# Optimization experiments

Measured on AMD Instinct MI355X. Metric: run time of the kernel, lower is better.

The kernel has to match this reference:

```python
import jax, jax.numpy as jnp
import numpy as np

B, N, D = 8, 2048, 512

def setup_inputs() -> dict:
    key = jax.random.key(0)
    ks = jax.random.split(key, 8)
    s = 1.0 / np.sqrt(D)
    return {
        "inputs": jax.random.normal(ks[0], (B, N, D), dtype=jnp.float32),
        "mask": jnp.ones((B, N), dtype=jnp.int32),
        "Wk": jax.random.normal(ks[1], (D, D), dtype=jnp.float32) * s,
        "bk": jax.random.normal(ks[2], (D,), dtype=jnp.float32) * s,
        "Wq": jax.random.normal(ks[3], (D, D), dtype=jnp.float32) * s,
        "bq": jax.random.normal(ks[4], (D,), dtype=jnp.float32) * s,
        "Wv": jax.random.normal(ks[5], (D, D), dtype=jnp.float32) * s,
        "bv": jax.random.normal(ks[6], (D,), dtype=jnp.float32) * s,
    }

def reference(inputs, mask, Wk, bk, Wq, bq, Wv, bv):
    # torch Linear: y = x @ W.T + b
    keys = jnp.einsum('bnd,ed->bne', inputs, Wk) + bk
    queries = jnp.einsum('bnd,ed->bne', inputs, Wq) + bq
    values = jnp.einsum('bnd,ed->bne', inputs, Wv) + bv
    norm = jnp.sqrt(jnp.asarray(D, inputs.dtype))
    scores = jnp.einsum('bqd,bkd->bqk', queries, keys) / norm  # [B,N,N]
    scores = jnp.where(mask[:, None, :] == 0, jnp.asarray(-1e9, scores.dtype), scores)
    attn = jax.nn.softmax(scores, axis=-1)
    return jnp.einsum('bqk,bkd->bqd', attn, values)
```

## Files before the change

kernel.cpp:

```cpp
#include <hip/hip_runtime.h>
#include <hip/hip_bf16.h>


typedef __attribute__((ext_vector_type(8))) short short8;
typedef __attribute__((ext_vector_type(4))) float f32x4;

#define DEV __device__ __forceinline__
#define GLOBAL_AS __attribute__((address_space(1)))
#define LDS_AS __attribute__((address_space(3)))

static DEV ushort f2bs(float f) {
  union { float f; unsigned u; } x; x.f = f;
  unsigned r = (x.u + 0x7fffu + ((x.u >> 16) & 1u)) >> 16;
  return (ushort)r;
}

static DEV f32x4 mfma16(short8 a, short8 b, f32x4 c) {
  return __builtin_amdgcn_mfma_f32_16x16x32_bf16(a, b, c, 0, 0, 0);
}

static DEV void async16(const void* g, void* l) {
  __builtin_amdgcn_global_load_lds((const GLOBAL_AS void*)g, (LDS_AS void*)l, 16, 0, 0);
}

__global__ void convert_all(const float* __restrict__ wq, const float* __restrict__ wk,
                            const float* __restrict__ wv, const float* __restrict__ x,
                            ushort* __restrict__ wb, ushort* __restrict__ xb,
                            float* __restrict__ lde) {
  int i = blockIdx.x * 256 + threadIdx.x;
  if (i >= 2293760) {
    int off = (i - 2293760) * 4;
    float4 z; z.x = 0.f; z.y = 0.f; z.z = 0.f; z.w = 0.f;
    *(float4*)(lde + off) = z;
    return;
  }
  const float* src;
  ushort* dst;
  if (i < 196608) {
    int which = i >> 16;
    int off = (i & 65535) * 4;
    src = ((which == 0) ? wq : (which == 1) ? wk : wv) + off;
    dst = wb + (size_t)which * 262144 + off;
  } else {
    int off = (i - 196608) * 4;
    src = x + off;
    dst = xb + off;
  }
  float4 v = *(const float4*)src;
  ushort4 o;
  o.x = f2bs(v.x); o.y = f2bs(v.y); o.z = f2bs(v.z); o.w = f2bs(v.w);
  *(ushort4*)dst = o;
}

#define KLOOP_STAGE(Aptr, lda, Bptr, ldb)                                      \
  do {                                                                         \
    _Pragma("unroll")                                                          \
    for (int t = 0; t < 8; t++) {                                              \
      int rowbase = (t & 3) * 32 + wave * 8;                                   \
      int r = rowbase + (lane >> 3);                                           \
      int gc = (lane & 7) ^ (r & 7);                                           \
      if (t < 4)                                                               \
        async16((Aptr) + (size_t)(rowblk * 128 + r) * (lda) + kb + gc * 8,     \
                &As[rowbase * 64]);                                            \
      else                                                                     \
        async16((Bptr) + (size_t)(colblk * 128 + r) * (ldb) + kb + gc * 8,     \
                &Bs[rowbase * 64]);                                            \
    }                                                                          \
  } while (0)

#define KLOOP_MFMA()                                                           \
  do {                                                                         \
    _Pragma("unroll")                                                          \
    for (int ks = 0; ks < 2; ks++) {                                           \
      short8 af[4], bfr[4];                                                    \
      _Pragma("unroll")                                                        \
      for (int t = 0; t < 4; t++) {                                            \
        int ra = wm * 64 + t * 16 + c16;                                       \
        int rb = wn * 64 + t * 16 + c16;                                       \
        af[t]  = *(const short8*)&As[ra * 64 + (((ks * 4 + quad) ^ (ra & 7)) * 8)]; \
        bfr[t] = *(const short8*)&Bs[rb * 64 + (((ks * 4 + quad) ^ (rb & 7)) * 8)]; \
      }                                                                        \
      _Pragma("unroll")                                                        \
      for (int mt = 0; mt < 4; mt++)                                           \
        _Pragma("unroll")                                                      \
        for (int nt = 0; nt < 4; nt++)                                         \
          acc[mt][nt] = mfma16(af[mt], bfr[nt], acc[mt][nt]);                  \
    }                                                                          \
  } while (0)

__launch_bounds__(256, 4)
__global__ void qkv_gemm(const ushort* __restrict__ Xb, const ushort* __restrict__ Wb,
                         const float* __restrict__ bq, const float* __restrict__ bk,
                         const float* __restrict__ bv,
                         ushort* __restrict__ Qb, ushort* __restrict__ Kb,
                         ushort* __restrict__ Vtb) {
  const int rowblk = blockIdx.x;
  const int colblk = blockIdx.y;
  const int z = colblk >> 2;

  __shared__ ushort S[2 * 128 * 64];
  ushort* As = S;
  ushort* Bs = S + 128 * 64;

  const int tid = threadIdx.x;
  const int wave = tid >> 6, lane = tid & 63, quad = lane >> 4, c16 = lane & 15;
  const int wm = wave & 1, wn = wave >> 1;

  f32x4 acc[4][4];
#pragma unroll
  for (int mt = 0; mt < 4; mt++)
#pragma unroll
    for (int nt = 0; nt < 4; nt++) acc[mt][nt] = (f32x4)0.0f;

  for (int kb = 0; kb < 512; kb += 64) {
    __syncthreads();
    KLOOP_STAGE(Xb, 512, Wb, 512);
    __syncthreads();
    KLOOP_MFMA();
  }

  const float* bias = (z == 0) ? bq : (z == 1) ? bk : bv;
  float bvals[4];
#pragma unroll
  for (int nt = 0; nt < 4; nt++) {
    int eg = colblk * 128 + wn * 64 + nt * 16 + c16;
    bvals[nt] = bias[eg & 511];
  }
  const float sc = (z == 0) ? 0.044194173824159216f : 1.0f;

  const int row0 = rowblk * 128 + wm * 64;
  const int col0 = colblk * 128 + wn * 64;
  if (z < 2) {
    ushort* O = (z == 0) ? Qb : Kb;
#pragma unroll
    for (int mt = 0; mt < 4; mt++)
#pragma unroll
      for (int nt = 0; nt < 4; nt++) {
        int el = (col0 + nt * 16 + c16) & 511;
#pragma unroll
        for (int r = 0; r < 4; r++) {
          int n = row0 + mt * 16 + quad * 4 + r;
          O[(size_t)n * 512 + el] = f2bs((acc[mt][nt][r] + bvals[nt]) * sc);
        }
      }
  } else {
    __syncthreads();
    ushort* T = S;
#pragma unroll
    for (int nt = 0; nt < 4; nt++) {
      int ell = wn * 64 + nt * 16 + c16;
#pragma unroll
      for (int mt = 0; mt < 4; mt++) {
        int n0l = wm * 64 + mt * 16 + quad * 4;
        ushort4 o;
        o.x = f2bs(acc[mt][nt][0] + bvals[nt]);
        o.y = f2bs(acc[mt][nt][1] + bvals[nt]);
        o.z = f2bs(acc[mt][nt][2] + bvals[nt]);
        o.w = f2bs(acc[mt][nt][3] + bvals[nt]);
        *(ushort4*)&T[ell * 128 + (((n0l >> 3) ^ (ell & 15)) << 3) + (n0l & 4)] = o;
      }
    }
    __syncthreads();
    const int c4 = tid & 3, er = tid >> 2;
    const int bb = rowblk >> 4;
    const int nbase = (rowblk & 15) * 128;
    const int elbase = (colblk & 3) * 128;
#pragma unroll
    for (int part = 0; part < 2; part++) {
      int ell = part * 64 + er;
      size_t ge = ((size_t)bb * 512 + elbase + ell) * 2048;
#pragma unroll
      for (int j2 = 0; j2 < 4; j2++) {
        int n0 = j2 * 32 + c4 * 8;
        short8 v = *(short8*)&T[ell * 128 + (((n0 >> 3) ^ (ell & 15)) << 3)];
        __builtin_nontemporal_store(v, (short8*)(Vtb + ge + nbase + n0));
      }
    }
  }
}

__launch_bounds__(256, 4)
__global__ void gemm_s(const ushort* __restrict__ Kb, const ushort* __restrict__ Qb,
                       const int* __restrict__ mask, ushort* __restrict__ Pm,
                       float* __restrict__ l) {
  const int bid = blockIdx.x;
  const int b = bid & 7;
  const int rowblk = (bid >> 3) & 15;
  const int colblk = bid >> 7;
  const ushort* A  = Kb + (size_t)b * 2048 * 512;
  const ushort* Bq = Qb + (size_t)b * 2048 * 512;

  __shared__ ushort S[2 * 128 * 64];
  ushort* As = S;
  ushort* Bs = S + 128 * 64;

  const int tid = threadIdx.x;
  const int wave = tid >> 6, lane = tid & 63, quad = lane >> 4, c16 = lane & 15;
  const int wm = wave & 1, wn = wave >> 1;

  f32x4 acc[4][4];
#pragma unroll
  for (int mt = 0; mt < 4; mt++)
#pragma unroll
    for (int nt = 0; nt < 4; nt++) acc[mt][nt] = (f32x4)0.0f;

  for (int kb = 0; kb < 512; kb += 64) {
    __syncthreads();
    KLOOP_STAGE(A, 512, Bq, 512);
    __syncthreads();
    KLOOP_MFMA();
  }

  const int row0 = rowblk * 128 + wm * 64;
  const int col0 = colblk * 128 + wn * 64;
  float lpart[4] = {0.0f, 0.0f, 0.0f, 0.0f};

  __syncthreads();
  ushort* T = S;
#pragma unroll
  for (int mt = 0; mt < 4; mt++) {
    int key0 = row0 + mt * 16 + quad * 4;
    int k0l  = wm * 64 + mt * 16 + quad * 4;
    int4 mv = *(const int4*)&mask[b * 2048 + key0];
    float mf0 = mv.x ? 1.0f : 0.0f, mf1 = mv.y ? 1.0f : 0.0f;
    float mf2 = mv.z ? 1.0f : 0.0f, mf3 = mv.w ? 1.0f : 0.0f;
#pragma unroll
    for (int nt = 0; nt < 4; nt++) {
      int ql = wn * 64 + nt * 16 + c16;
      float p0 = __expf(acc[mt][nt][0]) * mf0;
      float p1 = __expf(acc[mt][nt][1]) * mf1;
      float p2 = __expf(acc[mt][nt][2]) * mf2;
      float p3 = __expf(acc[mt][nt][3]) * mf3;
      ushort4 o;
      o.x = f2bs(p0); o.y = f2bs(p1); o.z = f2bs(p2); o.w = f2bs(p3);
      *(ushort4*)&T[ql * 128 + (((k0l >> 3) ^ (ql & 15)) << 3) + (k0l & 4)] = o;
      lpart[nt] += p0 + p1 + p2 + p3;
    }
  }
#pragma unroll
  for (int nt = 0; nt < 4; nt++) {
    float v = lpart[nt];
    v += __shfl_xor(v, 16, 64);
    v += __shfl_xor(v, 32, 64);
    if (quad == 0) atomicAdd(&l[b * 2048 + col0 + nt * 16 + c16], v);
  }
  __syncthreads();
  {
    const int c4 = tid & 3, er = tid >> 2;
#pragma unroll
    for (int part = 0; part < 2; part++) {
      int ql = part * 64 + er;
      size_t gq = ((size_t)b * 2048 + colblk * 128 + ql) * 2048;
#pragma unroll
      for (int j2 = 0; j2 < 4; j2++) {
        int n0 = j2 * 32 + c4 * 8;
        short8 v = *(short8*)&T[ql * 128 + (((n0 >> 3) ^ (ql & 15)) << 3)];
        __builtin_nontemporal_store(v, (short8*)(Pm + gq + rowblk * 128 + n0));
      }
    }
  }
}

#define PH_ST_A(pp, kt, rd)                                                    \
  do {                                                                         \
    int rowbase_ = (rd) * 64 + wave * 8;                                       \
    int r_ = rowbase_ + (lane >> 3);                                           \
    int gc_ = (lane & 7) ^ (r_ & 7);                                           \
    async16(gA + (size_t)(arow0 + r_) * glda + (kt) * 64 + gc_ * 8,            \
            SdA + (pp) * 16384 + rowbase_ * 64);                               \
  } while (0)

#define PH_ST_B(pp, kt, rd)                                                    \
  do {                                                                         \
    int rowbase_ = (rd) * 64 + wave * 8;                                       \
    int r_ = rowbase_ + (lane >> 3);                                           \
    int gc_ = (lane & 7) ^ (r_ & 7);                                           \
    async16(gB + (size_t)(brow0 + r_) * gldb + (kt) * 64 + gc_ * 8,            \
            SdB + (pp) * 8192 + rowbase_ * 64);                                \
  } while (0)

#define PH_READ(pp, ks, afx, bfx)                                              \
  do {                                                                         \
    const ushort* Ap_ = SdA + (pp) * 16384;                                    \
    const ushort* Bp_ = SdB + (pp) * 8192;                                     \
    _Pragma("unroll")                                                          \
    for (int mf = 0; mf < 4; mf++) {                                           \
      int ra = wm * 64 + mf * 16 + c16;                                        \
      afx[mf] = *(const short8*)&Ap_[ra * 64 + ((((ks)*4 + quad) ^ (ra & 7)) * 8)]; \
    }                                                                          \
    _Pragma("unroll")                                                          \
    for (int nf = 0; nf < 4; nf++) {                                           \
      int rb = wn * 64 + nf * 16 + c16;                                        \
      bfx[nf] = *(const short8*)&Bp_[rb * 64 + ((((ks)*4 + quad) ^ (rb & 7)) * 8)]; \
    }                                                                          \
  } while (0)

#define PH_MFMA(afx, bfx, h)                                                   \
  do {                                                                         \
    __builtin_amdgcn_s_setprio(1);                                             \
    _Pragma("unroll")                                                          \
    for (int mf = (h) * 2; mf < (h) * 2 + 2; mf++)                             \
      _Pragma("unroll")                                                        \
      for (int nf = 0; nf < 4; nf++)                                           \
        acc[mf][nf] = mfma16(afx[mf], bfx[nf], acc[mf][nf]);                   \
    __builtin_amdgcn_s_setprio(0);                                             \
  } while (0)

#define PH_TILE(pp, kt, dostage)                                               \
  do {                                                                         \
    PH_READ(pp, 0, af0, bf0);                                                  \
    __builtin_amdgcn_s_barrier();                                              \
    asm volatile("s_waitcnt lgkmcnt(0)" ::: "memory");                         \
    __builtin_amdgcn_sched_barrier(0);                                         \
    PH_MFMA(af0, bf0, 0);                                                      \
    __builtin_amdgcn_s_barrier();                                              \
    PH_READ(pp, 1, af1, bf1);                                                  \
    __builtin_amdgcn_s_barrier();                                              \
    asm volatile("s_waitcnt lgkmcnt(0)" ::: "memory");                         \
    __builtin_amdgcn_sched_barrier(0);                                         \
    PH_MFMA(af0, bf0, 1);                                                      \
    __builtin_amdgcn_s_barrier();         \
    if (dostage) { PH_ST_A(pp, (kt) + 2, 0); PH_ST_A(pp, (kt) + 2, 1);         \
                   PH_ST_A(pp, (kt) + 2, 2); }                                 \
    PH_MFMA(af1, bf1, 0);                                                      \
    __builtin_amdgcn_s_barrier();                                              \
    if (dostage) { PH_ST_A(pp, (kt) + 2, 3); PH_ST_B(pp, (kt) + 2, 0);         \
                   PH_ST_B(pp, (kt) + 2, 1); }                                 \
    PH_MFMA(af1, bf1, 1);                                                      \
    if (dostage) { asm volatile("s_waitcnt vmcnt(6)" ::: "memory"); }          \
    else         { asm volatile("s_waitcnt vmcnt(0)" ::: "memory"); }          \
    __builtin_amdgcn_sched_barrier(0);                                         \
    __builtin_amdgcn_s_barrier();        \
  } while (0)

#define PH_PROLOGUE()                                                          \
  do {                                                                         \
    PH_ST_A(0, 0, 0); PH_ST_A(0, 0, 1); PH_ST_A(0, 0, 2); PH_ST_A(0, 0, 3);    \
    PH_ST_B(0, 0, 0); PH_ST_B(0, 0, 1);                                        \
    PH_ST_A(1, 1, 0); PH_ST_A(1, 1, 1); PH_ST_A(1, 1, 2); PH_ST_A(1, 1, 3);    \
    PH_ST_B(1, 1, 0); PH_ST_B(1, 1, 1);                                        \
    asm volatile("s_waitcnt vmcnt(6)" ::: "memory");                           \
    __builtin_amdgcn_sched_barrier(0);                                         \
    __builtin_amdgcn_s_barrier();                                              \
  } while (0)

__launch_bounds__(512, 2)
__global__ void gemm_o(const ushort* __restrict__ Pm, const ushort* __restrict__ Vtb,
                       const float* __restrict__ l, float* __restrict__ out) {
  const int bid = blockIdx.x;
  const int b = bid & 7;
  const int rowblk = (bid >> 3) & 7;
  const int colblk = bid >> 6;

  extern __shared__ ushort Sd[];
  ushort* SdA = Sd;
  ushort* SdB = Sd + 32768;

  const int tid = threadIdx.x;
  const int wave = tid >> 6, lane = tid & 63, quad = lane >> 4, c16 = lane & 15;
  const int wm = wave >> 1, wn = wave & 1;

  const ushort* gA = Pm + (size_t)b * 2048 * 2048;  const int glda = 2048;
  const int arow0 = rowblk * 256;
  const ushort* gB = Vtb + (size_t)b * 512 * 2048;  const int gldb = 2048;
  const int brow0 = colblk * 128;

  f32x4 acc[4][4];
#pragma unroll
  for (int mf = 0; mf < 4; mf++)
#pragma unroll
    for (int nf = 0; nf < 4; nf++) acc[mf][nf] = (f32x4)0.0f;

  PH_PROLOGUE();
  short8 af0[4], bf0[4], af1[4], bf1[4];
  for (int i = 0; i < 16; i++) {
    const int ds = (i < 15);
    PH_TILE(0, 2 * i, ds);
    PH_TILE(1, 2 * i + 1, ds);
  }

  const int row0 = rowblk * 256 + wm * 64;
  const int col0 = colblk * 128 + wn * 64;
  float linv[4][4];
#pragma unroll
  for (int mf = 0; mf < 4; mf++)
#pragma unroll
    for (int r = 0; r < 4; r++)
      linv[mf][r] = 1.0f / l[b * 2048 + row0 + mf * 16 + quad * 4 + r];
#pragma unroll
  for (int mf = 0; mf < 4; mf++)
#pragma unroll
    for (int nf = 0; nf < 4; nf++) {
      int col = col0 + nf * 16 + c16;
#pragma unroll
      for (int r = 0; r < 4; r++) {
        int row = row0 + mf * 16 + quad * 4 + r;
        out[((size_t)b * 2048 + row) * 512 + col] = acc[mf][nf][r] * linv[mf][r];
      }
    }
}

extern "C" void kernel_launch(void* const* d_in, const int* in_sizes, int n_in,
                              void* d_out, int out_size, void* d_ws, size_t ws_size,
                              hipStream_t stream) {
  (void)in_sizes; (void)n_in; (void)out_size; (void)ws_size;
  const float* X    = (const float*)d_in[0];
  const int*   mask = (const int*)d_in[1];
  const float* Wk   = (const float*)d_in[2];
  const float* bk   = (const float*)d_in[3];
  const float* Wq   = (const float*)d_in[4];
  const float* bq   = (const float*)d_in[5];
  const float* Wv   = (const float*)d_in[6];
  const float* bv   = (const float*)d_in[7];
  float* out = (float*)d_out;

  ushort* ws  = (ushort*)d_ws;
  ushort* Pm  = ws;
  ushort* Xb  = ws;
  ushort* Wb  = ws + (size_t)33554432;
  ushort* Qb  = Wb + (size_t)786432;
  ushort* Kb  = Qb + (size_t)8388608;
  ushort* Vtb = Kb + (size_t)8388608;
  float*  lde = (float*)(Vtb + (size_t)8388608);

  convert_all<<<8976, 256, 0, stream>>>(Wq, Wk, Wv, X, Wb, Xb, lde);
  qkv_gemm<<<dim3(128, 12), 256, 0, stream>>>(Xb, Wb, bq, bk, bv, Qb, Kb, Vtb);
  gemm_s<<<2048, 256, 0, stream>>>(Kb, Qb, mask, Pm, lde);
  gemm_o<<<256, 512, 98304, stream>>>(Pm, Vtb, lde, out);
}
```

Baseline: 197.4 us.

## Triple-buffer LDS pipeline in output GEMM with deeper prefetch

Converts the gemm_o main loop from double to triple buffering in shared memory, prefetching tile k+3 instead of k+2. It adds a three-stage prologue, unrolled loop tail handling and a final tile with no barrier. The intent is to hide more global-load latency behind MFMA work. In exchange, dynamic LDS grows to 144KB, which limits residency to one block per CU.

```diff
diff --git a/kernel.cpp b/kernel.cpp
--- a/kernel.cpp
+++ b/kernel.cpp
@@ -306,7 +306,10 @@
     __builtin_amdgcn_s_setprio(0);                                             \
   } while (0)
 
-#define PH_TILE(pp, kt, dostage)                                               \
+#define PH_WAIT_(N) asm volatile("s_waitcnt vmcnt(" #N ")" ::: "memory")
+#define PH_WAIT(N) PH_WAIT_(N)
+
+#define PH_TILE3(pp, kt, dostage, WN)                                          \
   do {                                                                         \
     PH_READ(pp, 0, af0, bf0);                                                  \
     __builtin_amdgcn_s_barrier();                                              \
@@ -320,26 +323,43 @@
     __builtin_amdgcn_sched_barrier(0);                                         \
     PH_MFMA(af0, bf0, 1);                                                      \
     __builtin_amdgcn_s_barrier();         \
-    if (dostage) { PH_ST_A(pp, (kt) + 2, 0); PH_ST_A(pp, (kt) + 2, 1);         \
-                   PH_ST_A(pp, (kt) + 2, 2); }                                 \
+    if (dostage) { PH_ST_A(pp, (kt) + 3, 0); PH_ST_A(pp, (kt) + 3, 1);         \
+                   PH_ST_A(pp, (kt) + 3, 2); }                                 \
     PH_MFMA(af1, bf1, 0);                                                      \
     __builtin_amdgcn_s_barrier();                                              \
-    if (dostage) { PH_ST_A(pp, (kt) + 2, 3); PH_ST_B(pp, (kt) + 2, 0);         \
-                   PH_ST_B(pp, (kt) + 2, 1); }                                 \
+    if (dostage) { PH_ST_A(pp, (kt) + 3, 3); PH_ST_B(pp, (kt) + 3, 0);         \
+                   PH_ST_B(pp, (kt) + 3, 1); }                                 \
     PH_MFMA(af1, bf1, 1);                                                      \
-    if (dostage) { asm volatile("s_waitcnt vmcnt(6)" ::: "memory"); }          \
-    else         { asm volatile("s_waitcnt vmcnt(0)" ::: "memory"); }          \
+    PH_WAIT(WN);                                                               \
     __builtin_amdgcn_sched_barrier(0);                                         \
     __builtin_amdgcn_s_barrier();        \
   } while (0)
 
-#define PH_PROLOGUE()                                                          \
+#define PH_TILE3_LAST(pp)                                                      \
+  do {                                                                         \
+    PH_READ(pp, 0, af0, bf0);                                                  \
+    __builtin_amdgcn_s_barrier();                                              \
+    asm volatile("s_waitcnt lgkmcnt(0)" ::: "memory");                         \
+    __builtin_amdgcn_sched_barrier(0);                                         \
+    PH_MFMA(af0, bf0, 0);                                                      \
+    __builtin_amdgcn_s_barrier();                                              \
+    PH_READ(pp, 1, af1, bf1);                                                  \
+    asm volatile("s_waitcnt lgkmcnt(0)" ::: "memory");                         \
+    __builtin_amdgcn_sched_barrier(0);                                         \
+    PH_MFMA(af0, bf0, 1);                                                      \
+    PH_MFMA(af1, bf1, 0);                                                      \
+    PH_MFMA(af1, bf1, 1);                                                      \
+  } while (0)
+
+#define PH_PROLOGUE3()                                                         \
   do {                                                                         \
     PH_ST_A(0, 0, 0); PH_ST_A(0, 0, 1); PH_ST_A(0, 0, 2); PH_ST_A(0, 0, 3);    \
     PH_ST_B(0, 0, 0); PH_ST_B(0, 0, 1);                                        \
     PH_ST_A(1, 1, 0); PH_ST_A(1, 1, 1); PH_ST_A(1, 1, 2); PH_ST_A(1, 1, 3);    \
     PH_ST_B(1, 1, 0); PH_ST_B(1, 1, 1);                                        \
-    asm volatile("s_waitcnt vmcnt(6)" ::: "memory");                           \
+    PH_ST_A(2, 2, 0); PH_ST_A(2, 2, 1); PH_ST_A(2, 2, 2); PH_ST_A(2, 2, 3);    \
+    PH_ST_B(2, 2, 0); PH_ST_B(2, 2, 1);                                        \
+    PH_WAIT(12);                                                               \
     __builtin_amdgcn_sched_barrier(0);                                         \
     __builtin_amdgcn_s_barrier();                                              \
   } while (0)
@@ -354,7 +374,7 @@
 
   extern __shared__ ushort Sd[];
   ushort* SdA = Sd;
-  ushort* SdB = Sd + 32768;
+  ushort* SdB = Sd + 3 * 16384;
 
   const int tid = threadIdx.x;
   const int wave = tid >> 6, lane = tid & 63, quad = lane >> 4, c16 = lane & 15;
@@ -371,13 +391,18 @@
 #pragma unroll
     for (int nf = 0; nf < 4; nf++) acc[mf][nf] = (f32x4)0.0f;
 
-  PH_PROLOGUE();
+  PH_PROLOGUE3();
   short8 af0[4], bf0[4], af1[4], bf1[4];
-  for (int i = 0; i < 16; i++) {
-    const int ds = (i < 15);
-    PH_TILE(0, 2 * i, ds);
-    PH_TILE(1, 2 * i + 1, ds);
-  }
+  for (int i = 0; i < 9; i++) {
+    PH_TILE3(0, 3 * i,     1, 12);
+    PH_TILE3(1, 3 * i + 1, 1, 12);
+    PH_TILE3(2, 3 * i + 2, 1, 12);
+  }
+  PH_TILE3(0, 27, 1, 12);
+  PH_TILE3(1, 28, 1, 12);
+  PH_TILE3(2, 29, 0, 6);
+  PH_TILE3(0, 30, 0, 0);
+  PH_TILE3_LAST(1);
 
   const int row0 = rowblk * 256 + wm * 64;
   const int col0 = colblk * 128 + wn * 64;
@@ -426,5 +451,5 @@
   convert_all<<<8976, 256, 0, stream>>>(Wq, Wk, Wv, X, Wb, Xb, lde);
   qkv_gemm<<<dim3(128, 12), 256, 0, stream>>>(Xb, Wb, bq, bk, bv, Qb, Kb, Vtb);
   gemm_s<<<2048, 256, 0, stream>>>(Kb, Qb, mask, Pm, lde);
-  gemm_o<<<256, 512, 98304, stream>>>(Pm, Vtb, lde, out);
-}
+  gemm_o<<<256, 512, 147456, stream>>>(Pm, Vtb, lde, out);
+}
```

Result: slower. 202.5 us (median of 2 runs) (+2.6%).
